# Performance work log

Hardware: AMD Instinct MI355X
Metric: run time of the kernel (lower is better)

The kernel has to match this reference:

```python
import jax, jax.numpy as jnp
import numpy as np

EMB = 1024
DM = 64
NH = 16

def setup_inputs() -> dict:
    key = jax.random.key(0)
    ks = jax.random.split(key, 11)
    bs, slen = 2, 2048
    s = 1.0 / np.sqrt(EMB)
    inp = {
        'Q': jax.random.normal(ks[0], (bs, slen, EMB), jnp.float32),
        'K': jax.random.normal(ks[1], (bs, slen, EMB), jnp.float32),
        'V': jax.random.normal(ks[2], (bs, slen, EMB), jnp.float32),
        'Wq': jax.random.normal(ks[3], (EMB, DM * NH), jnp.float32) * s,
        'bq': jnp.zeros((DM * NH,), jnp.float32),
        'Wk': jax.random.normal(ks[4], (EMB, DM * NH), jnp.float32) * s,
        'bk': jnp.zeros((DM * NH,), jnp.float32),
        'Wv': jax.random.normal(ks[5], (EMB, DM * NH), jnp.float32) * s,
        'bv': jnp.zeros((DM * NH,), jnp.float32),
        'Wo': jax.random.normal(ks[6], (DM * NH, EMB), jnp.float32) * (1.0 / np.sqrt(DM * NH)),
        'bo': jnp.zeros((EMB,), jnp.float32),
    }
    return inp

def reference(Q, K, V, Wq, bq, Wk, bk, Wv, bv, Wo, bo):
    bs, q_len, _ = Q.shape
    kv_len = K.shape[1]
    scale = 1.0 / np.sqrt(DM)
    # project and split heads: (n, l, h, d)
    q = (scale * (Q @ Wq + bq)).reshape(bs, q_len, NH, DM)
    k = (K @ Wk + bk).reshape(bs, kv_len, NH, DM)
    v = (V @ Wv + bv).reshape(bs, kv_len, NH, DM)
    # scores (n, h, l, s) -- full S x S matrix, as in the original
    qk = jnp.einsum('nlhd,nshd->nhls', q, k)
    a = jax.nn.softmax(qk, axis=-1)  # dropout p=0 -> identity
    o = jnp.einsum('nhls,nshd->nlhd', a, v).reshape(bs, q_len, NH * DM)
    return o @ Wo + bo
```

## Files before the change

### kernel.cpp

```cpp
#include <hip/hip_runtime.h>
#include <cstdint>
#include <cstddef>

#define EMB  1024
#define DM   64
#define NH   16
#define SLEN 2048
#define BS   2

typedef _Float16 f16x8 __attribute__((ext_vector_type(8)));
typedef _Float16 f16x4 __attribute__((ext_vector_type(4)));
typedef __fp16   hf2   __attribute__((ext_vector_type(2)));
typedef __fp16   hf4   __attribute__((ext_vector_type(4)));
typedef __fp16   hf8   __attribute__((ext_vector_type(8)));
typedef float    f32x4 __attribute__((ext_vector_type(4)));

#define ASYNC_LD16(gp, lp)                                                        \
    __builtin_amdgcn_global_load_lds(                                             \
        (const __attribute__((address_space(1))) void*)(gp),                      \
        (__attribute__((address_space(3))) void*)(lp), 16, 0, 0)

__global__ __launch_bounds__(256)
void prep(const float* __restrict__ Q, const float* __restrict__ K,
          const float* __restrict__ V,
          const float* __restrict__ Wq, const float* __restrict__ Wk,
          const float* __restrict__ Wv, const float* __restrict__ Wo,
          _Float16* __restrict__ Qh, _Float16* __restrict__ Kh,
          _Float16* __restrict__ Vh,
          _Float16* __restrict__ WqT, _Float16* __restrict__ WkT,
          _Float16* __restrict__ WvT, _Float16* __restrict__ WoT)
{
    __shared__ float t[64][65];
    const int z = blockIdx.z;
    if (z < 3) {
        const float* in  = (z == 0) ? Q : (z == 1) ? K : V;
        _Float16*    out = (z == 0) ? Qh : (z == 1) ? Kh : Vh;
        size_t i = ((size_t)blockIdx.x * 256 + threadIdx.x) * 8;
        float4 a = *(const float4*)(in + i);
        float4 b = *(const float4*)(in + i + 4);
        f16x8 o;
        o[0] = (_Float16)a.x; o[1] = (_Float16)a.y; o[2] = (_Float16)a.z; o[3] = (_Float16)a.w;
        o[4] = (_Float16)b.x; o[5] = (_Float16)b.y; o[6] = (_Float16)b.z; o[7] = (_Float16)b.w;
        *(f16x8*)(out + i) = o;
        return;
    }
    if (blockIdx.x >= 256) return;
    const float* W;
    _Float16*    T;
    switch (z - 3) {
        case 0:  W = Wq; T = WqT; break;
        case 1:  W = Wk; T = WkT; break;
        case 2:  W = Wv; T = WvT; break;
        default: W = Wo; T = WoT; break;
    }
    const int tid = threadIdx.x;
    const int bn  = (blockIdx.x & 15) * 64;
    const int bk  = (blockIdx.x >> 4) * 64;

    #pragma unroll
    for (int p = 0; p < 4; ++p) {
        int row = p * 16 + (tid >> 4);
        int col = (tid & 15) * 4;
        float4 v = *(const float4*)(W + (size_t)(bk + row) * EMB + bn + col);
        t[row][col+0] = v.x; t[row][col+1] = v.y; t[row][col+2] = v.z; t[row][col+3] = v.w;
    }
    __syncthreads();
    #pragma unroll
    for (int p = 0; p < 4; ++p) {
        int nr = p * 16 + (tid >> 4);
        int kc = (tid & 15) * 4;
        f16x4 o;
        o[0] = (_Float16)t[kc+0][nr];
        o[1] = (_Float16)t[kc+1][nr];
        o[2] = (_Float16)t[kc+2][nr];
        o[3] = (_Float16)t[kc+3][nr];
        *(f16x4*)&T[(size_t)(bn + nr) * EMB + bk + kc] = o;
    }
}

__device__ __forceinline__
void gemm_core(const _Float16* __restrict__ A, const _Float16* __restrict__ Bt,
               const float* __restrict__ bias, float* __restrict__ Cf,
               _Float16* __restrict__ Ch, int M, int N, int K,
               float scale, int mode, int bx, int by)
{
    __shared__ __align__(16) _Float16 As[128 * 32];
    __shared__ __align__(16) _Float16 Bs[128 * 32];

    const int tid  = threadIdx.x;
    const int lane = tid & 63;
    const int wave = tid >> 6;
    const int c    = lane & 15;
    const int quad = lane >> 4;
    const int bm   = by * 128;
    const int bn   = bx * 128;
    const int wm   = (wave >> 1) * 64;
    const int wn   = (wave & 1) * 64;

    f32x4 acc[4][4];
    #pragma unroll
    for (int i = 0; i < 4; ++i)
        #pragma unroll
        for (int j = 0; j < 4; ++j)
            #pragma unroll
            for (int r = 0; r < 4; ++r) acc[i][j][r] = 0.f;

    const char* gA = (const char*)(A + (size_t)(bm + (tid >> 2)) * K) + (tid & 3) * 16;
    const char* gB = (const char*)(Bt + (size_t)(bn + (tid >> 2)) * K) + (tid & 3) * 16;
    char* lA = (char*)As + wave * 1024;
    char* lB = (char*)Bs + wave * 1024;
    const size_t rowskip = (size_t)64 * K * 2;

    for (int k0 = 0; k0 < K; k0 += 32) {
        __syncthreads();
        ASYNC_LD16(gA + (size_t)k0 * 2,           lA);
        ASYNC_LD16(gA + rowskip + (size_t)k0 * 2, lA + 4096);
        ASYNC_LD16(gB + (size_t)k0 * 2,           lB);
        ASYNC_LD16(gB + rowskip + (size_t)k0 * 2, lB + 4096);
        __syncthreads();

        f16x8 af[4], bf[4];
        #pragma unroll
        for (int i = 0; i < 4; ++i)
            af[i] = *(const f16x8*)&As[(wm + i * 16 + c) * 32 + quad * 8];
        #pragma unroll
        for (int j = 0; j < 4; ++j)
            bf[j] = *(const f16x8*)&Bs[(wn + j * 16 + c) * 32 + quad * 8];

        #pragma unroll
        for (int i = 0; i < 4; ++i)
            #pragma unroll
            for (int j = 0; j < 4; ++j)
                acc[i][j] = __builtin_amdgcn_mfma_f32_16x16x32_f16(af[i], bf[j], acc[i][j], 0, 0, 0);
    }

    float bcol[4];
    #pragma unroll
    for (int j = 0; j < 4; ++j) bcol[j] = bias[bn + wn + j * 16 + c];

    #pragma unroll
    for (int i = 0; i < 4; ++i) {
        int m0 = bm + wm + i * 16 + quad * 4;
        #pragma unroll
        for (int j = 0; j < 4; ++j) {
            int n = bn + wn + j * 16 + c;
            if (mode == 0) {
                #pragma unroll
                for (int r = 0; r < 4; ++r)
                    Cf[(size_t)(m0 + r) * N + n] = acc[i][j][r] + bcol[j];
            } else if (mode == 1) {
                int h = n >> 6, d = n & 63;
                #pragma unroll
                for (int r = 0; r < 4; ++r) {
                    int mm = m0 + r;
                    int b = mm >> 11, l = mm & (SLEN - 1);
                    Ch[(((size_t)(b * NH + h)) * SLEN + l) * DM + d] =
                        (_Float16)((acc[i][j][r] + bcol[j]) * scale);
                }
            } else {
                int h = n >> 6, d = n & 63;
                int b = m0 >> 11, l = m0 & (SLEN - 1);
                f16x4 o;
                #pragma unroll
                for (int r = 0; r < 4; ++r)
                    o[r] = (_Float16)(acc[i][j][r] + bcol[j]);
                *(f16x4*)&Ch[(((size_t)(b * NH + h)) * DM + d) * SLEN + l] = o;
            }
        }
    }
}

__global__ __launch_bounds__(256)
void gemm_qkv(const _Float16* __restrict__ Qh, const _Float16* __restrict__ Kh,
              const _Float16* __restrict__ Vh,
              const _Float16* __restrict__ WqT, const _Float16* __restrict__ WkT,
              const _Float16* __restrict__ WvT,
              const float* __restrict__ bq, const float* __restrict__ bk,
              const float* __restrict__ bv,
              _Float16* __restrict__ q_ws, _Float16* __restrict__ k_ws,
              _Float16* __restrict__ v_ws)
{
    const _Float16 *A, *Bt;
    const float* bias;
    _Float16* Ch;
    float scale;
    int mode;
    if (blockIdx.z == 0)      { A = Qh; Bt = WqT; bias = bq; Ch = q_ws; scale = 0.18033688f; mode = 1; }
    else if (blockIdx.z == 1) { A = Kh; Bt = WkT; bias = bk; Ch = k_ws; scale = 1.0f;        mode = 1; }
    else                      { A = Vh; Bt = WvT; bias = bv; Ch = v_ws; scale = 1.0f;        mode = 2; }
    gemm_core(A, Bt, bias, nullptr, Ch, BS * SLEN, NH * DM, EMB, scale, mode,
              blockIdx.x, blockIdx.y);
}

__global__ __launch_bounds__(256)
void gemm_out(const _Float16* __restrict__ Oh, const _Float16* __restrict__ WoT,
              const float* __restrict__ bo, float* __restrict__ out)
{
    gemm_core(Oh, WoT, bo, out, nullptr, BS * SLEN, EMB, NH * DM, 1.0f, 0,
              blockIdx.x, blockIdx.y);
}

__global__ __launch_bounds__(256)
void attn_mfma(const _Float16* __restrict__ qw, const _Float16* __restrict__ kw,
               const _Float16* __restrict__ vwT, _Float16* __restrict__ ow)
{
    __shared__ __align__(16) _Float16 Kt[2][64 * 64];
    __shared__ __align__(16) _Float16 Vt[2][64 * 64];

    const int tid  = threadIdx.x;
    const int lane = tid & 63;
    const int wave = tid >> 6;
    const int c    = lane & 15;
    const int quad = lane >> 4;
    const int bh   = blockIdx.y;
    const int b    = bh >> 4;
    const int h    = bh & 15;
    const int qbase = blockIdx.x * 128 + wave * 32;

    const _Float16* kb = kw  + (size_t)bh * SLEN * DM;
    const _Float16* vb = vwT + (size_t)bh * DM * SLEN;
    const _Float16* qb = qw  + (size_t)bh * SLEN * DM;

    f16x8 qf[2][2];
    #pragma unroll
    for (int t = 0; t < 2; ++t)
        #pragma unroll
        for (int ch = 0; ch < 2; ++ch)
            qf[t][ch] = *(const f16x8*)(qb + (size_t)(qbase + t*16 + c) * DM + ch*32 + quad*8);

    f32x4 oacc[2][4];
    f32x4 lacc[2];
    #pragma unroll
    for (int t = 0; t < 2; ++t) {
        #pragma unroll
        for (int dg = 0; dg < 4; ++dg)
            #pragma unroll
            for (int r = 0; r < 4; ++r) oacc[t][dg][r] = 0.f;
        #pragma unroll
        for (int r = 0; r < 4; ++r) lacc[t][r] = 0.f;
    }
    const f16x8 ones8 = {(_Float16)1.f, (_Float16)1.f, (_Float16)1.f, (_Float16)1.f,
                         (_Float16)1.f, (_Float16)1.f, (_Float16)1.f, (_Float16)1.f};
    const f32x4 zero4 = {0.f, 0.f, 0.f, 0.f};

    const int r0  = wave * 16 + (lane >> 3);
    const int lc0 = (((lane & 7) ^ (r0 & 7)) * 16);
    const char* gk = (const char*)kb + r0 * 128 + lc0;
    const char* gv = (const char*)vb + (size_t)r0 * 4096 + lc0;
    char* lK = (char*)&Kt[0][0] + wave * 2048;
    char* lV = (char*)&Vt[0][0] + wave * 2048;

    ASYNC_LD16(gk,         lK);
    ASYNC_LD16(gk + 1024,  lK + 1024);
    ASYNC_LD16(gv,         lV);
    ASYNC_LD16(gv + 32768, lV + 1024);
    gk += 8192; gv += 128;
    __syncthreads();

    auto tile = [&](int cur) {
        {
            char* pk = (char*)&Kt[cur ^ 1][0] + wave * 2048;
            char* pv = (char*)&Vt[cur ^ 1][0] + wave * 2048;
            ASYNC_LD16(gk,         pk);
            ASYNC_LD16(gk + 1024,  pk + 1024);
            ASYNC_LD16(gv,         pv);
            ASYNC_LD16(gv + 32768, pv + 1024);
            gk += 8192; gv += 128;
        }

        f16x8 kf[4][2];
        #pragma unroll
        for (int g = 0; g < 4; ++g)
            #pragma unroll
            for (int ch = 0; ch < 2; ++ch)
                kf[g][ch] = *(const f16x8*)
                    &Kt[cur][(g*16 + c) * 64 + (((ch*4 + quad) ^ (c & 7)) * 8)];

        f32x4 s[2][4];
        #pragma unroll
        for (int t = 0; t < 2; ++t)
            #pragma unroll
            for (int g = 0; g < 4; ++g) {
                s[t][g] = __builtin_amdgcn_mfma_f32_16x16x32_f16(kf[g][0], qf[t][0], zero4,   0, 0, 0);
                s[t][g] = __builtin_amdgcn_mfma_f32_16x16x32_f16(kf[g][1], qf[t][1], s[t][g], 0, 0, 0);
            }

        f16x8 pf8[2][2];
        #pragma unroll
        for (int t = 0; t < 2; ++t)
            #pragma unroll
            for (int kk = 0; kk < 2; ++kk) {
                hf4 h4[2];
                #pragma unroll
                for (int u = 0; u < 2; ++u) {
                    float p0 = __builtin_amdgcn_exp2f(s[t][2*kk + u][0]);
                    float p1 = __builtin_amdgcn_exp2f(s[t][2*kk + u][1]);
                    float p2 = __builtin_amdgcn_exp2f(s[t][2*kk + u][2]);
                    float p3 = __builtin_amdgcn_exp2f(s[t][2*kk + u][3]);
                    hf2 lo = __builtin_amdgcn_cvt_pkrtz(p0, p1);
                    hf2 hi = __builtin_amdgcn_cvt_pkrtz(p2, p3);
                    h4[u] = __builtin_shufflevector(lo, hi, 0, 1, 2, 3);
                }
                hf8 h8 = __builtin_shufflevector(h4[0], h4[1], 0, 1, 2, 3, 4, 5, 6, 7);
                pf8[t][kk] = __builtin_bit_cast(f16x8, h8);
            }

        #pragma unroll
        for (int kk = 0; kk < 2; ++kk) {
            lacc[0] = __builtin_amdgcn_mfma_f32_16x16x32_f16(pf8[0][kk], ones8, lacc[0], 0, 0, 0);
            lacc[1] = __builtin_amdgcn_mfma_f32_16x16x32_f16(pf8[1][kk], ones8, lacc[1], 0, 0, 0);
        }

        #pragma unroll
        for (int dg = 0; dg < 4; ++dg) {
            f16x4 vf[4];
            #pragma unroll
            for (int g = 0; g < 4; ++g)
                vf[g] = *(const f16x4*)
                    &Vt[cur][(dg*16 + c) * 64 +
                             (((2*g + (quad >> 1)) ^ (c & 7)) * 8) + (quad & 1) * 4];
            f16x8 v01 = __builtin_shufflevector(vf[0], vf[1], 0, 1, 2, 3, 4, 5, 6, 7);
            f16x8 v23 = __builtin_shufflevector(vf[2], vf[3], 0, 1, 2, 3, 4, 5, 6, 7);
            #pragma unroll
            for (int t = 0; t < 2; ++t) {
                oacc[t][dg] = __builtin_amdgcn_mfma_f32_16x16x32_f16(pf8[t][0], v01, oacc[t][dg], 0, 0, 0);
                oacc[t][dg] = __builtin_amdgcn_mfma_f32_16x16x32_f16(pf8[t][1], v23, oacc[t][dg], 0, 0, 0);
            }
        }
        __syncthreads();
    };

    for (int it = 0; it < SLEN / 64; it += 2) {
        tile(0);
        tile(1);
    }

    #pragma unroll
    for (int t = 0; t < 2; ++t) {
        #pragma unroll
        for (int r = 0; r < 4; ++r) {
            float linv = 1.0f / lacc[t][r];
            int row = qbase + t*16 + quad*4 + r;
            #pragma unroll
            for (int dg = 0; dg < 4; ++dg)
                ow[((size_t)b * SLEN + row) * EMB + h * DM + dg*16 + c] =
                    (_Float16)(oacc[t][dg][r] * linv);
        }
    }
}

extern "C" void kernel_launch(void* const* d_in, const int* in_sizes, int n_in,
                              void* d_out, int out_size, void* d_ws, size_t ws_size,
                              hipStream_t stream)
{
    const float* Q  = (const float*)d_in[0];
    const float* K  = (const float*)d_in[1];
    const float* V  = (const float*)d_in[2];
    const float* Wq = (const float*)d_in[3];
    const float* bq = (const float*)d_in[4];
    const float* Wk = (const float*)d_in[5];
    const float* bk = (const float*)d_in[6];
    const float* Wv = (const float*)d_in[7];
    const float* bv = (const float*)d_in[8];
    const float* Wo = (const float*)d_in[9];
    const float* bo = (const float*)d_in[10];
    float* out = (float*)d_out;

    const size_t MN = (size_t)BS * SLEN * NH * DM;
    const size_t WW = (size_t)EMB * NH * DM;

    _Float16* base = (_Float16*)d_ws;
    _Float16* Qh   = base;
    _Float16* Kh   = Qh  + MN;
    _Float16* Vh   = Kh  + MN;
    _Float16* WqT  = Vh  + MN;
    _Float16* WkT  = WqT + WW;
    _Float16* WvT  = WkT + WW;
    _Float16* WoT  = WvT + WW;
    _Float16* q_ws = WoT + WW;
    _Float16* k_ws = q_ws + MN;
    _Float16* v_ws = k_ws + MN;
    _Float16* o_ws = v_ws + MN;

    dim3 blk(256);

    prep<<<dim3(2048, 1, 7), blk, 0, stream>>>(Q, K, V, Wq, Wk, Wv, Wo,
                                               Qh, Kh, Vh, WqT, WkT, WvT, WoT);

    gemm_qkv<<<dim3(8, 32, 3), blk, 0, stream>>>(Qh, Kh, Vh, WqT, WkT, WvT,
                                                 bq, bk, bv, q_ws, k_ws, v_ws);

    attn_mfma<<<dim3(SLEN / 128, BS * NH), blk, 0, stream>>>(q_ws, k_ws, v_ws, o_ws);

    gemm_out<<<dim3(8, 32, 1), blk, 0, stream>>>(o_ws, WoT, bo, out);
}
```

Baseline: 228.1 us.

## Split attention block into 8 waves of 16 query rows each

The attention kernel now launches 512 threads per block, and each of the 8 waves handles 16 query rows instead of 32. The K/V tile loads are spread across more waves, so each lane issues one async load per tile for K and one for V. The aim is to cut per-wave register pressure and increase the number of waves available to hide MFMA and LDS latency. The cost is that each K/V fragment read from LDS is reused across half as many query rows, which doubles LDS read traffic per unit of compute.

After: 232.3 us. About the same (+1.8%).

```diff
diff --git a/kernel.cpp b/kernel.cpp
--- a/kernel.cpp
+++ b/kernel.cpp
@@ -200,7 +200,7 @@
               blockIdx.x, blockIdx.y);
 }
 
-__global__ __launch_bounds__(256)
+__global__ __launch_bounds__(512)
 void attn_mfma(const _Float16* __restrict__ qw, const _Float16* __restrict__ kw,
                const _Float16* __restrict__ vwT, _Float16* __restrict__ ow)
 {
@@ -215,56 +215,48 @@
     const int bh   = blockIdx.y;
     const int b    = bh >> 4;
     const int h    = bh & 15;
-    const int qbase = blockIdx.x * 128 + wave * 32;
+    const int qbase = blockIdx.x * 128 + wave * 16;
 
     const _Float16* kb = kw  + (size_t)bh * SLEN * DM;
     const _Float16* vb = vwT + (size_t)bh * DM * SLEN;
     const _Float16* qb = qw  + (size_t)bh * SLEN * DM;
 
-    f16x8 qf[2][2];
-    #pragma unroll
-    for (int t = 0; t < 2; ++t)
-        #pragma unroll
-        for (int ch = 0; ch < 2; ++ch)
-            qf[t][ch] = *(const f16x8*)(qb + (size_t)(qbase + t*16 + c) * DM + ch*32 + quad*8);
-
-    f32x4 oacc[2][4];
-    f32x4 lacc[2];
-    #pragma unroll
-    for (int t = 0; t < 2; ++t) {
-        #pragma unroll
-        for (int dg = 0; dg < 4; ++dg)
-            #pragma unroll
-            for (int r = 0; r < 4; ++r) oacc[t][dg][r] = 0.f;
-        #pragma unroll
-        for (int r = 0; r < 4; ++r) lacc[t][r] = 0.f;
-    }
+    f16x8 qf[2];
+    #pragma unroll
+    for (int ch = 0; ch < 2; ++ch)
+        qf[ch] = *(const f16x8*)(qb + (size_t)(qbase + c) * DM + ch*32 + quad*8);
+
+    f32x4 oacc[4];
+    f32x4 lacc;
+    #pragma unroll
+    for (int dg = 0; dg < 4; ++dg)
+        #pragma unroll
+        for (int r = 0; r < 4; ++r) oacc[dg][r] = 0.f;
+    #pragma unroll
+    for (int r = 0; r < 4; ++r) lacc[r] = 0.f;
+
     const f16x8 ones8 = {(_Float16)1.f, (_Float16)1.f, (_Float16)1.f, (_Float16)1.f,
                          (_Float16)1.f, (_Float16)1.f, (_Float16)1.f, (_Float16)1.f};
     const f32x4 zero4 = {0.f, 0.f, 0.f, 0.f};
 
-    const int r0  = wave * 16 + (lane >> 3);
-    const int lc0 = (((lane & 7) ^ (r0 & 7)) * 16);
+    const int r0  = wave * 8 + (lane >> 3);
+    const int lc0 = (((lane & 7) ^ ((lane >> 3) & 7)) * 16);
     const char* gk = (const char*)kb + r0 * 128 + lc0;
     const char* gv = (const char*)vb + (size_t)r0 * 4096 + lc0;
-    char* lK = (char*)&Kt[0][0] + wave * 2048;
-    char* lV = (char*)&Vt[0][0] + wave * 2048;
-
-    ASYNC_LD16(gk,         lK);
-    ASYNC_LD16(gk + 1024,  lK + 1024);
-    ASYNC_LD16(gv,         lV);
-    ASYNC_LD16(gv + 32768, lV + 1024);
+    char* lK = (char*)&Kt[0][0] + wave * 1024;
+    char* lV = (char*)&Vt[0][0] + wave * 1024;
+
+    ASYNC_LD16(gk, lK);
+    ASYNC_LD16(gv, lV);
     gk += 8192; gv += 128;
     __syncthreads();
 
     auto tile = [&](int cur) {
         {
-            char* pk = (char*)&Kt[cur ^ 1][0] + wave * 2048;
-            char* pv = (char*)&Vt[cur ^ 1][0] + wave * 2048;
-            ASYNC_LD16(gk,         pk);
-            ASYNC_LD16(gk + 1024,  pk + 1024);
-            ASYNC_LD16(gv,         pv);
-            ASYNC_LD16(gv + 32768, pv + 1024);
+            char* pk = (char*)&Kt[cur ^ 1][0] + wave * 1024;
+            char* pv = (char*)&Vt[cur ^ 1][0] + wave * 1024;
+            ASYNC_LD16(gk, pk);
+            ASYNC_LD16(gv, pv);
             gk += 8192; gv += 128;
         }
 
@@ -276,40 +268,34 @@
                 kf[g][ch] = *(const f16x8*)
                     &Kt[cur][(g*16 + c) * 64 + (((ch*4 + quad) ^ (c & 7)) * 8)];
 
-        f32x4 s[2][4];
-        #pragma unroll
-        for (int t = 0; t < 2; ++t)
-            #pragma unroll
-            for (int g = 0; g < 4; ++g) {
-                s[t][g] = __builtin_amdgcn_mfma_f32_16x16x32_f16(kf[g][0], qf[t][0], zero4,   0, 0, 0);
-                s[t][g] = __builtin_amdgcn_mfma_f32_16x16x32_f16(kf[g][1], qf[t][1], s[t][g], 0, 0, 0);
+        f32x4 s[4];
+        #pragma unroll
+        for (int g = 0; g < 4; ++g) {
+            s[g] = __builtin_amdgcn_mfma_f32_16x16x32_f16(kf[g][0], qf[0], zero4, 0, 0, 0);
+            s[g] = __builtin_amdgcn_mfma_f32_16x16x32_f16(kf[g][1], qf[1], s[g],  0, 0, 0);
+        }
+
+        f16x8 pf8[2];
+        #pragma unroll
+        for (int kk = 0; kk < 2; ++kk) {
+            hf4 h4[2];
+            #pragma unroll
+            for (int u = 0; u < 2; ++u) {
+                float p0 = __builtin_amdgcn_exp2f(s[2*kk + u][0]);
+                float p1 = __builtin_amdgcn_exp2f(s[2*kk + u][1]);
+                float p2 = __builtin_amdgcn_exp2f(s[2*kk + u][2]);
+                float p3 = __builtin_amdgcn_exp2f(s[2*kk + u][3]);
+                hf2 lo = __builtin_amdgcn_cvt_pkrtz(p0, p1);
+                hf2 hi = __builtin_amdgcn_cvt_pkrtz(p2, p3);
+                h4[u] = __builtin_shufflevector(lo, hi, 0, 1, 2, 3);
             }
-
-        f16x8 pf8[2][2];
-        #pragma unroll
-        for (int t = 0; t < 2; ++t)
-            #pragma unroll
-            for (int kk = 0; kk < 2; ++kk) {
-                hf4 h4[2];
-                #pragma unroll
-                for (int u = 0; u < 2; ++u) {
-                    float p0 = __builtin_amdgcn_exp2f(s[t][2*kk + u][0]);
-                    float p1 = __builtin_amdgcn_exp2f(s[t][2*kk + u][1]);
-                    float p2 = __builtin_amdgcn_exp2f(s[t][2*kk + u][2]);
-                    float p3 = __builtin_amdgcn_exp2f(s[t][2*kk + u][3]);
-                    hf2 lo = __builtin_amdgcn_cvt_pkrtz(p0, p1);
-                    hf2 hi = __builtin_amdgcn_cvt_pkrtz(p2, p3);
-                    h4[u] = __builtin_shufflevector(lo, hi, 0, 1, 2, 3);
-                }
-                hf8 h8 = __builtin_shufflevector(h4[0], h4[1], 0, 1, 2, 3, 4, 5, 6, 7);
-                pf8[t][kk] = __builtin_bit_cast(f16x8, h8);
-            }
-
-        #pragma unroll
-        for (int kk = 0; kk < 2; ++kk) {
-            lacc[0] = __builtin_amdgcn_mfma_f32_16x16x32_f16(pf8[0][kk], ones8, lacc[0], 0, 0, 0);
-            lacc[1] = __builtin_amdgcn_mfma_f32_16x16x32_f16(pf8[1][kk], ones8, lacc[1], 0, 0, 0);
-        }
+            hf8 h8 = __builtin_shufflevector(h4[0], h4[1], 0, 1, 2, 3, 4, 5, 6, 7);
+            pf8[kk] = __builtin_bit_cast(f16x8, h8);
+        }
+
+        #pragma unroll
+        for (int kk = 0; kk < 2; ++kk)
+            lacc = __builtin_amdgcn_mfma_f32_16x16x32_f16(pf8[kk], ones8, lacc, 0, 0, 0);
 
         #pragma unroll
         for (int dg = 0; dg < 4; ++dg) {
@@ -321,11 +307,8 @@
                              (((2*g + (quad >> 1)) ^ (c & 7)) * 8) + (quad & 1) * 4];
             f16x8 v01 = __builtin_shufflevector(vf[0], vf[1], 0, 1, 2, 3, 4, 5, 6, 7);
             f16x8 v23 = __builtin_shufflevector(vf[2], vf[3], 0, 1, 2, 3, 4, 5, 6, 7);
-            #pragma unroll
-            for (int t = 0; t < 2; ++t) {
-                oacc[t][dg] = __builtin_amdgcn_mfma_f32_16x16x32_f16(pf8[t][0], v01, oacc[t][dg], 0, 0, 0);
-                oacc[t][dg] = __builtin_amdgcn_mfma_f32_16x16x32_f16(pf8[t][1], v23, oacc[t][dg], 0, 0, 0);
-            }
+            oacc[dg] = __builtin_amdgcn_mfma_f32_16x16x32_f16(pf8[0], v01, oacc[dg], 0, 0, 0);
+            oacc[dg] = __builtin_amdgcn_mfma_f32_16x16x32_f16(pf8[1], v23, oacc[dg], 0, 0, 0);
         }
         __syncthreads();
     };
@@ -336,16 +319,13 @@
     }
 
     #pragma unroll
-    for (int t = 0; t < 2; ++t) {
-        #pragma unroll
-        for (int r = 0; r < 4; ++r) {
-            float linv = 1.0f / lacc[t][r];
-            int row = qbase + t*16 + quad*4 + r;
-            #pragma unroll
-            for (int dg = 0; dg < 4; ++dg)
-                ow[((size_t)b * SLEN + row) * EMB + h * DM + dg*16 + c] =
-                    (_Float16)(oacc[t][dg][r] * linv);
-        }
+    for (int r = 0; r < 4; ++r) {
+        float linv = 1.0f / lacc[r];
+        int row = qbase + quad*4 + r;
+        #pragma unroll
+        for (int dg = 0; dg < 4; ++dg)
+            ow[((size_t)b * SLEN + row) * EMB + h * DM + dg*16 + c] =
+                (_Float16)(oacc[dg][r] * linv);
     }
 }
 
@@ -390,7 +370,7 @@
     gemm_qkv<<<dim3(8, 32, 3), blk, 0, stream>>>(Qh, Kh, Vh, WqT, WkT, WvT,
                                                  bq, bk, bv, q_ws, k_ws, v_ws);
 
-    attn_mfma<<<dim3(SLEN / 128, BS * NH), blk, 0, stream>>>(q_ws, k_ws, v_ws, o_ws);
+    attn_mfma<<<dim3(SLEN / 128, BS * NH), dim3(512), 0, stream>>>(q_ws, k_ws, v_ws, o_ws);
 
     gemm_out<<<dim3(8, 32, 1), blk, 0, stream>>>(o_ws, WoT, bo, out);
 }
```
